# Performance work log

Hardware: AMD Instinct MI355X
Metric: run time of the kernel (lower is better)

The kernel has to match this reference:

```python
import jax, jax.numpy as jnp
import numpy as np

B, N, KNN, C, H, LK, CEMB, GDIM = 16, 512, 20, 256, 128, 4, 64, 64


def _lrelu(x, slope):
    return jnp.where(x >= 0, x, slope * x)


def _forward(img_feat, graph_feat, roi_mask_bit, prev_x_id, prev_y_id, knn_idx,
             conv_w, conv_b, pre_w1, pre_b1, pre_w2, pre_b2,
             g1_w, g1_gamma, g1_beta, g1_mean, g1_var,
             g2_w, g2_gamma, g2_beta, g2_mean, g2_var,
             q_w1, q_b1, q_w2, q_b2, q_w3, q_b3):
    lk = conv_w.shape[-1]
    bsz = img_feat.shape[0]
    # Index2Feat: conv with padding = lk-1 -> (B, CEMB, H+lk-1, W+lk-1)
    patches = jax.lax.conv_general_dilated(img_feat, conv_w, (1, 1), [(lk - 1, lk - 1)] * 2)
    patches = patches + conv_b[None, :, None, None]
    p = jnp.transpose(patches, (0, 2, 3, 1))  # (B, Hp, Wp, CEMB)
    bi = jnp.arange(bsz)[:, None]
    yy, xx = 2 * prev_y_id, 2 * prev_x_id
    sf1 = p[bi, yy, xx]
    sf2 = p[bi, yy + lk, xx]
    sf3 = p[bi, yy, xx + lk]
    sf4 = p[bi, yy + lk, xx + lk]
    local = jnp.concatenate([sf1, sf2, sf3, sf4], axis=-1)  # (B, N, 4*CEMB)
    local = local * jnp.transpose(roi_mask_bit, (0, 2, 1))  # detached mask
    local = jnp.concatenate([local, jnp.transpose(graph_feat, (0, 2, 1))], axis=-1)  # (B,N,320)
    # pre_graph MLP (LeakyReLU 0.01, doLastAct=True)
    h = _lrelu(local @ pre_w1 + pre_b1, 0.01)
    h = _lrelu(h @ pre_w2 + pre_b2, 0.01)  # (B, N, C)
    knn = knn_idx[0]  # (N, K) shared across batch

    def edgeconv(x, w, gamma, beta, mean, var):
        xk = x[:, knn]  # (B, N, K, C) neighbor gather
        xc = jnp.broadcast_to(x[:, :, None, :], xk.shape)
        e = jnp.concatenate([xk - xc, xc], axis=-1)  # (B, N, K, 2C)
        y = jnp.einsum('bnkc,oc->bnko', e, w)  # 1x1 conv, no bias
        y = (y - mean) * (gamma / jnp.sqrt(var + 1e-5)) + beta  # BN (inference)
        return _lrelu(y, 0.2).max(axis=2)  # max over k neighbors

    h = edgeconv(h, g1_w, g1_gamma, g1_beta, g1_mean, g1_var)
    h = edgeconv(h, g2_w, g2_gamma, g2_beta, g2_mean, g2_var)
    # query MLP (256 -> 256 -> 64 -> 2), LeakyReLU 0.01, no last act
    q = _lrelu(h @ q_w1 + q_b1, 0.01)
    q = _lrelu(q @ q_w2 + q_b2, 0.01)
    bits = q @ q_w3 + q_b3  # (B, N, 2)
    return jnp.transpose(bits, (0, 2, 1)), jnp.transpose(h, (0, 2, 1))


def setup_inputs() -> dict:
    key = jax.random.key(0)
    ks = jax.random.split(key, 24)
    s = 0.02
    img_feat = jax.random.normal(ks[0], (B, C, H, H), jnp.float32)
    graph_feat = jax.random.normal(ks[1], (B, GDIM, N), jnp.float32)
    roi_mask_bit = jnp.ones((B, 1, N), jnp.float32)
    prev_x_id = jax.random.randint(ks[2], (B, N), 0, H // 2, jnp.int32)
    prev_y_id = jax.random.randint(ks[3], (B, N), 0, H // 2, jnp.int32)
    # knn graph from normalized 3D keypoints (computed once at init in torch)
    p3d = jax.random.uniform(ks[4], (1, 3, N), jnp.float32, -1.0, 1.0)
    inner = -2.0 * jnp.einsum('bdn,bdm->bnm', p3d, p3d)
    xsq = jnp.sum(p3d ** 2, axis=1, keepdims=True)  # (1,1,N)
    pd = -xsq - inner - jnp.transpose(xsq, (0, 2, 1))
    knn_idx = jax.lax.top_k(pd, KNN)[1].astype(jnp.int32)  # (1, N, KNN)
    return {
        'img_feat': img_feat, 'graph_feat': graph_feat, 'roi_mask_bit': roi_mask_bit,
        'prev_x_id': prev_x_id, 'prev_y_id': prev_y_id, 'knn_idx': knn_idx,
        'conv_w': jax.random.normal(ks[5], (CEMB, C, LK, LK), jnp.float32) * s,
        'conv_b': jnp.zeros((CEMB,), jnp.float32),
        'pre_w1': jax.random.normal(ks[6], (4 * CEMB + GDIM, C), jnp.float32) * s,
        'pre_b1': jnp.zeros((C,), jnp.float32),
        'pre_w2': jax.random.normal(ks[7], (C, C), jnp.float32) * s,
        'pre_b2': jnp.zeros((C,), jnp.float32),
        'g1_w': jax.random.normal(ks[8], (C, 2 * C), jnp.float32) * s,
        'g1_gamma': jnp.ones((C,), jnp.float32), 'g1_beta': jnp.zeros((C,), jnp.float32),
        'g1_mean': jnp.zeros((C,), jnp.float32), 'g1_var': jnp.ones((C,), jnp.float32),
        'g2_w': jax.random.normal(ks[9], (C, 2 * C), jnp.float32) * s,
        'g2_gamma': jnp.ones((C,), jnp.float32), 'g2_beta': jnp.zeros((C,), jnp.float32),
        'g2_mean': jnp.zeros((C,), jnp.float32), 'g2_var': jnp.ones((C,), jnp.float32),
        'q_w1': jax.random.normal(ks[10], (C, C), jnp.float32) * s,
        'q_b1': jnp.zeros((C,), jnp.float32),
        'q_w2': jax.random.normal(ks[11], (C, 64), jnp.float32) * s,
        'q_b2': jnp.zeros((64,), jnp.float32),
        'q_w3': jax.random.normal(ks[12], (64, 2), jnp.float32) * s,
        'q_b3': jnp.zeros((2,), jnp.float32),
    }


def reference(img_feat, graph_feat, roi_mask_bit, prev_x_id, prev_y_id, knn_idx,
              conv_w, conv_b, pre_w1, pre_b1, pre_w2, pre_b2,
              g1_w, g1_gamma, g1_beta, g1_mean, g1_var,
              g2_w, g2_gamma, g2_beta, g2_mean, g2_var,
              q_w1, q_b1, q_w2, q_b2, q_w3, q_b3):
    return _forward(img_feat, graph_feat, roi_mask_bit, prev_x_id, prev_y_id, knn_idx,
                    conv_w, conv_b, pre_w1, pre_b1, pre_w2, pre_b2,
                    g1_w, g1_gamma, g1_beta, g1_mean, g1_var,
                    g2_w, g2_gamma, g2_beta, g2_mean, g2_var,
                    q_w1, q_b1, q_w2, q_b2, q_w3, q_b3)
```

## Files before the change

### kernel.cpp

```cpp
#include <hip/hip_runtime.h>


typedef __bf16 bf16_t;
typedef bf16_t bf16x2 __attribute__((ext_vector_type(2)));
typedef bf16_t bf16x8 __attribute__((ext_vector_type(8)));
typedef float  f32x4  __attribute__((ext_vector_type(4)));

static constexpr int BATCH = 16;
static constexpr int NPT   = 512;
static constexpr int PTS   = BATCH * NPT;
static constexpr int CONVM = PTS * 4;
static constexpr int CONVK = 4096;

static constexpr int PY_DIM = 136;
static constexpr size_t IMG_BSTRIDE = (size_t)PY_DIM * PY_DIM * 256;

static constexpr size_t OFF_WCONV_OLD = 0;
static constexpr size_t OFF_WCONVP    = OFF_WCONV_OLD + (size_t)64*4096*2;
static constexpr size_t OFF_WPRE1     = OFF_WCONVP    + (size_t)64*4096*2;
static constexpr size_t OFF_WPRE2     = OFF_WPRE1     + (size_t)256*320*2;
static constexpr size_t OFF_WEC1      = OFF_WPRE2     + (size_t)256*256*2;
static constexpr size_t OFF_WEC2      = OFF_WEC1      + (size_t)512*256*2;
static constexpr size_t OFF_WQ1       = OFF_WEC2      + (size_t)512*256*2;
static constexpr size_t OFF_WQ2       = OFF_WQ1       + (size_t)256*256*2;
static constexpr size_t OFF_LOCAL     = OFF_WQ2       + (size_t)64*256*2;
static constexpr size_t OFF_X         = OFF_LOCAL + (size_t)PTS*320*2;
static constexpr size_t OFF_Y         = OFF_X     + (size_t)PTS*256*2;
static constexpr size_t OFF_Z         = OFF_Y     + (size_t)PTS*256*2;
static constexpr size_t OFF_UNION     = OFF_Z     + (size_t)PTS*64*2;
static constexpr size_t AB_BYTES      = (size_t)PTS*512*4;
static constexpr size_t IMGT_BYTES    = (size_t)16*IMG_BSTRIDE*2;
static constexpr size_t WS_BASE       = OFF_UNION + AB_BYTES;
static constexpr size_t WS_FULL       = OFF_UNION + IMGT_BYTES;

static constexpr int WP_CONV  = 64*4096;
static constexpr int WP_CONVP = 64*4096;
static constexpr int WP_PRE1 = 256*320;
static constexpr int WP_PRE2 = 256*256;
static constexpr int WP_EC   = 512*256;
static constexpr int WP_Q1   = 256*256;
static constexpr int WP_Q2   = 64*256;
static constexpr int WP_TOTAL = WP_CONV + WP_CONVP + WP_PRE1 + WP_PRE2 + 2*WP_EC + WP_Q1 + WP_Q2;

__global__ __launch_bounds__(256) void wprep_kernel(
    const float* __restrict__ conv_w, const float* __restrict__ pre_w1,
    const float* __restrict__ pre_w2, const float* __restrict__ g1_w,
    const float* __restrict__ g2_w,   const float* __restrict__ q_w1,
    const float* __restrict__ q_w2,
    bf16_t* __restrict__ wt_conv, bf16_t* __restrict__ wt_convp,
    bf16_t* __restrict__ wt_pre1,
    bf16_t* __restrict__ wt_pre2, bf16_t* __restrict__ wt_ec1,
    bf16_t* __restrict__ wt_ec2,  bf16_t* __restrict__ wt_q1,
    bf16_t* __restrict__ wt_q2)
{
    int i = blockIdx.x * 256 + threadIdx.x;
    if (i >= WP_TOTAL) return;
    if (i < WP_CONV) { wt_conv[i] = (bf16_t)conv_w[i]; return; }
    i -= WP_CONV;
    if (i < WP_CONVP) {
        const int o = i >> 12, pix = (i >> 8) & 15, c = i & 255;
        wt_convp[i] = (bf16_t)conv_w[((o * 256 + c) << 4) + pix]; return; }
    i -= WP_CONVP;
    if (i < WP_PRE1) { int n = i / 320, k = i - n * 320;
        wt_pre1[i] = (bf16_t)pre_w1[k * 256 + n]; return; }
    i -= WP_PRE1;
    if (i < WP_PRE2) { int n = i >> 8, k = i & 255;
        wt_pre2[i] = (bf16_t)pre_w2[k * 256 + n]; return; }
    i -= WP_PRE2;
    if (i < WP_EC) { int n = i >> 8, k = i & 255;
        wt_ec1[i] = (bf16_t)(n < 256 ? g1_w[n * 512 + k] : g1_w[(n - 256) * 512 + 256 + k]);
        return; }
    i -= WP_EC;
    if (i < WP_EC) { int n = i >> 8, k = i & 255;
        wt_ec2[i] = (bf16_t)(n < 256 ? g2_w[n * 512 + k] : g2_w[(n - 256) * 512 + 256 + k]);
        return; }
    i -= WP_EC;
    if (i < WP_Q1) { int n = i >> 8, k = i & 255;
        wt_q1[i] = (bf16_t)q_w1[k * 256 + n]; return; }
    i -= WP_Q1;
    { int n = i >> 8, k = i & 255;
        wt_q2[i] = (bf16_t)q_w2[k * 64 + n]; }
}

static constexpr int PAD_THREADS = 16 * 2112 * 32;

__global__ __launch_bounds__(256) void pad_border(bf16_t* __restrict__ imgT)
{
    const int idx = blockIdx.x * 256 + threadIdx.x;
    if (idx >= PAD_THREADS) return;
    const int t = idx & 31;
    int pi = idx >> 5;
    const int b = pi / 2112; pi -= b * 2112;
    int y, x;
    if (pi < 544)      { y = pi / 136;              x = pi % 136; }
    else if (pi < 1088){ int j = pi - 544; y = 132 + j / 136; x = j % 136; }
    else { int j = pi - 1088; y = 4 + (j >> 3); int k = j & 7; x = (k < 4) ? k : (128 + k); }
    const uint4 z = {0, 0, 0, 0};
    ((uint4*)(imgT + ((size_t)(b * PY_DIM + y) * PY_DIM + x) * 256))[t] = z;
}

__global__ __launch_bounds__(256) void transpose_img(
    const float* __restrict__ img, bf16_t* __restrict__ imgT)
{
    __shared__ float T[64][65];
    const int bid = blockIdx.x;
    const int cc = bid & 3;
    const int xh = (bid >> 2) & 1;
    const int y  = (bid >> 3) & 127;
    const int b  = bid >> 10;
    const int t = threadIdx.x;
    const int x0 = xh * 64, c0 = cc * 64;
    {
        const int px = t & 63, cr = t >> 6;
        const float* src = img + ((size_t)(b * 256 + c0 + cr) * 128 + y) * 128 + x0 + px;
        #pragma unroll
        for (int i = 0; i < 16; ++i)
            T[cr + i * 4][px] = src[(size_t)i * 4 * 16384];
    }
    __syncthreads();
    {
        const int cl2 = (t & 31) * 2, pr = t >> 5;
        bf16_t* dst = imgT + ((size_t)(b * PY_DIM + y + 4) * PY_DIM + x0 + 4) * 256 + c0 + cl2;
        #pragma unroll
        for (int i = 0; i < 8; ++i) {
            const int pxl = pr + i * 8;
            bf16x2 w;
            w[0] = (bf16_t)T[cl2][pxl];
            w[1] = (bf16_t)T[cl2 + 1][pxl];
            *(bf16x2*)(dst + (size_t)pxl * 256) = w;
        }
    }
}

__global__ __launch_bounds__(256) void conv_gather_gemm3(
    const bf16_t* __restrict__ imgT,
    const bf16_t* __restrict__ Wc,
    const float* __restrict__ conv_b, const float* __restrict__ roi,
    const int* __restrict__ px, const int* __restrict__ py,
    bf16_t* __restrict__ local)
{
    __shared__ bf16_t As[32][136];
    __shared__ bf16_t Bs[64][136];
    const int tid = threadIdx.x, lane = tid & 63, wave = tid >> 6;
    const int wm = wave & 1, wn = wave >> 1;
    const int row0 = blockIdx.x * 32;

    const int ra = tid >> 3, seg = tid & 7;
    const int r = row0 + ra, corner = r & 3, pnt = r >> 2, b = pnt >> 9;
    const int oy = 2 * py[pnt] + (corner & 1) * 4 + 1;
    const int ox = 2 * px[pnt] + ((corner >> 1) & 1) * 4 + 1;
    const bf16_t* imgb = imgT + (size_t)b * IMG_BSTRIDE;
    const int rb = tid >> 2, sq = tid & 3;
    const bf16_t* wrow = Wc + (size_t)rb * 4096 + sq * 8;

    f32x4 acc[2] = {};
    #pragma unroll 1
    for (int s = 0; s < 32; ++s) {
        const int pix = s >> 1, h = s & 1;
        const int iy = oy + (pix >> 2), ix = ox + (pix & 3);
        {
            const bf16_t* srcA = imgb + ((size_t)(iy * PY_DIM + ix)) * 256 + h * 128 + seg * 16;
            *(uint4*)&As[ra][seg * 16]     = *(const uint4*)srcA;
            *(uint4*)&As[ra][seg * 16 + 8] = *(const uint4*)(srcA + 8);
        }
        {
            const bf16_t* srcB = wrow + pix * 256 + h * 128;
            #pragma unroll
            for (int i = 0; i < 4; ++i)
                *(uint4*)&Bs[rb][sq * 8 + i * 32] = *(const uint4*)(srcB + i * 32);
        }
        __syncthreads();
        #pragma unroll
        for (int kk = 0; kk < 128; kk += 32) {
            const int kf = kk + ((lane >> 4) << 3);
            bf16x8 a  = *(const bf16x8*)&As[wm * 16 + (lane & 15)][kf];
            bf16x8 b0 = *(const bf16x8*)&Bs[wn * 32 + (lane & 15)][kf];
            bf16x8 b1 = *(const bf16x8*)&Bs[wn * 32 + 16 + (lane & 15)][kf];
            acc[0] = __builtin_amdgcn_mfma_f32_16x16x32_bf16(a, b0, acc[0], 0, 0, 0);
            acc[1] = __builtin_amdgcn_mfma_f32_16x16x32_bf16(a, b1, acc[1], 0, 0, 0);
        }
        __syncthreads();
    }
    const int crow = (lane >> 4) << 2;
    const int ccol = lane & 15;
    #pragma unroll
    for (int j = 0; j < 2; ++j) {
        const int o = wn * 32 + j * 16 + ccol;
        const float bv = conv_b[o];
        #pragma unroll
        for (int rg = 0; rg < 4; ++rg) {
            const int gr = row0 + wm * 16 + crow + rg;
            const int cn = gr & 3;
            const int pp = gr >> 2;
            const float v = (acc[j][rg] + bv) * roi[pp];
            local[(size_t)pp * 320 + cn * 64 + o] = (bf16_t)v;
        }
    }
}

__global__ __launch_bounds__(256) void conv_gather_gemm(
    const float* __restrict__ img, const bf16_t* __restrict__ Wc,
    const float* __restrict__ conv_b, const float* __restrict__ roi,
    const int* __restrict__ px, const int* __restrict__ py,
    bf16_t* __restrict__ local)
{
    __shared__ bf16_t As[64][72];
    __shared__ bf16_t Bs[64][72];
    const int tid = threadIdx.x;
    const int lane = tid & 63;
    const int wave = tid >> 6;
    const int wm = wave & 1, wn = wave >> 1;
    const int row0 = blockIdx.x * 64;
    const int sm = tid >> 2;
    const int cq = tid & 3;
    const int r = row0 + sm;
    const int corner = r & 3;
    const int pnt = r >> 2;
    const int b = pnt >> 9;
    const int oy = 2 * py[pnt] + (corner & 1) * 4;
    const int ox = 2 * px[pnt] + ((corner >> 1) & 1) * 4;
    const int iy0 = oy - 3, ix0 = ox - 3;
    const float* imgb = img + (size_t)b * (256 * 128 * 128);

    f32x4 acc[2][2] = {};
    for (int kt = 0; kt < CONVK; kt += 64) {
        {
            const int c = (kt >> 4) + cq;
            const float* ip = imgb + (size_t)c * (128 * 128);
            alignas(16) bf16_t vals[16];
            #pragma unroll
            for (int ky = 0; ky < 4; ++ky) {
                const int iy = iy0 + ky;
                const bool yok = (unsigned)iy < 128u;
                #pragma unroll
                for (int kx = 0; kx < 4; ++kx) {
                    const int ix = ix0 + kx;
                    float v = (yok && (unsigned)ix < 128u) ? ip[iy * 128 + ix] : 0.0f;
                    vals[ky * 4 + kx] = (bf16_t)v;
                }
            }
            *(uint4*)&As[sm][cq * 16]     = *(const uint4*)&vals[0];
            *(uint4*)&As[sm][cq * 16 + 8] = *(const uint4*)&vals[8];
        }
        {
            const bf16_t* src = Wc + (size_t)sm * CONVK + kt + cq * 16;
            *(uint4*)&Bs[sm][cq * 16]     = *(const uint4*)src;
            *(uint4*)&Bs[sm][cq * 16 + 8] = *(const uint4*)(src + 8);
        }
        __syncthreads();
        #pragma unroll
        for (int kk = 0; kk < 64; kk += 32) {
            const int kf = kk + ((lane >> 4) << 3);
            bf16x8 a0 = *(const bf16x8*)&As[wm * 32 + (lane & 15)][kf];
            bf16x8 a1 = *(const bf16x8*)&As[wm * 32 + 16 + (lane & 15)][kf];
            bf16x8 b0 = *(const bf16x8*)&Bs[wn * 32 + (lane & 15)][kf];
            bf16x8 b1 = *(const bf16x8*)&Bs[wn * 32 + 16 + (lane & 15)][kf];
            acc[0][0] = __builtin_amdgcn_mfma_f32_16x16x32_bf16(a0, b0, acc[0][0], 0, 0, 0);
            acc[0][1] = __builtin_amdgcn_mfma_f32_16x16x32_bf16(a0, b1, acc[0][1], 0, 0, 0);
            acc[1][0] = __builtin_amdgcn_mfma_f32_16x16x32_bf16(a1, b0, acc[1][0], 0, 0, 0);
            acc[1][1] = __builtin_amdgcn_mfma_f32_16x16x32_bf16(a1, b1, acc[1][1], 0, 0, 0);
        }
        __syncthreads();
    }
    const int crow = (lane >> 4) << 2;
    const int ccol = lane & 15;
    #pragma unroll
    for (int i = 0; i < 2; ++i) {
        #pragma unroll
        for (int j = 0; j < 2; ++j) {
            const int o = wn * 32 + j * 16 + ccol;
            const float bv = conv_b[o];
            #pragma unroll
            for (int rg = 0; rg < 4; ++rg) {
                const int gr = row0 + wm * 32 + i * 16 + crow + rg;
                const int cn = gr & 3;
                const int pp = gr >> 2;
                const float v = (acc[i][j][rg] + bv) * roi[pp];
                local[(size_t)pp * 320 + cn * 64 + o] = (bf16_t)v;
            }
        }
    }
}

__global__ __launch_bounds__(256) void graph_fill(
    const float* __restrict__ g, bf16_t* __restrict__ local)
{
    const int e = blockIdx.x * 256 + threadIdx.x;
    const int j = e & 63, p = e >> 6;
    const int b = p >> 9, n = p & 511;
    local[(size_t)p * 320 + 256 + j] = (bf16_t)g[((size_t)(b * 64 + j) << 9) + n];
}

template<int K, int N, int ACT>
__global__ __launch_bounds__(256) void gemm_bf16(
    const bf16_t* __restrict__ A, const bf16_t* __restrict__ Bt,
    const float* __restrict__ bias, float slope,
    bf16_t* __restrict__ outB, float* __restrict__ outF)
{
    __shared__ bf16_t As[64][72];
    __shared__ bf16_t Bs[64][72];
    const int tid = threadIdx.x;
    const int lane = tid & 63;
    const int wave = tid >> 6;
    const int wm = wave & 1, wn = wave >> 1;
    const int row0 = blockIdx.x * 64;
    const int col0 = blockIdx.y * 64;
    const int sm = tid >> 2;
    const int sq = (tid & 3) << 4;

    f32x4 acc[2][2] = {};
    for (int kt = 0; kt < K; kt += 64) {
        {
            const bf16_t* src = A + (size_t)(row0 + sm) * K + kt + sq;
            *(uint4*)&As[sm][sq]     = *(const uint4*)src;
            *(uint4*)&As[sm][sq + 8] = *(const uint4*)(src + 8);
        }
        {
            const bf16_t* src = Bt + (size_t)(col0 + sm) * K + kt + sq;
            *(uint4*)&Bs[sm][sq]     = *(const uint4*)src;
            *(uint4*)&Bs[sm][sq + 8] = *(const uint4*)(src + 8);
        }
        __syncthreads();
        #pragma unroll
        for (int kk = 0; kk < 64; kk += 32) {
            const int kf = kk + ((lane >> 4) << 3);
            bf16x8 a0 = *(const bf16x8*)&As[wm * 32 + (lane & 15)][kf];
            bf16x8 a1 = *(const bf16x8*)&As[wm * 32 + 16 + (lane & 15)][kf];
            bf16x8 b0 = *(const bf16x8*)&Bs[wn * 32 + (lane & 15)][kf];
            bf16x8 b1 = *(const bf16x8*)&Bs[wn * 32 + 16 + (lane & 15)][kf];
            acc[0][0] = __builtin_amdgcn_mfma_f32_16x16x32_bf16(a0, b0, acc[0][0], 0, 0, 0);
            acc[0][1] = __builtin_amdgcn_mfma_f32_16x16x32_bf16(a0, b1, acc[0][1], 0, 0, 0);
            acc[1][0] = __builtin_amdgcn_mfma_f32_16x16x32_bf16(a1, b0, acc[1][0], 0, 0, 0);
            acc[1][1] = __builtin_amdgcn_mfma_f32_16x16x32_bf16(a1, b1, acc[1][1], 0, 0, 0);
        }
        __syncthreads();
    }
    const int crow = (lane >> 4) << 2;
    const int ccol = lane & 15;
    #pragma unroll
    for (int i = 0; i < 2; ++i) {
        #pragma unroll
        for (int j = 0; j < 2; ++j) {
            const int gcol = col0 + wn * 32 + j * 16 + ccol;
            const float bv = bias ? bias[gcol] : 0.0f;
            #pragma unroll
            for (int rg = 0; rg < 4; ++rg) {
                const int grow = row0 + wm * 32 + i * 16 + crow + rg;
                float v = acc[i][j][rg] + bv;
                if (ACT == 1) v = v >= 0.0f ? v : slope * v;
                if (outB) outB[(size_t)grow * N + gcol] = (bf16_t)v;
                if (outF) outF[(size_t)grow * N + gcol] = v;
            }
        }
    }
}

__global__ __launch_bounds__(256) void edge_combine(
    const float* __restrict__ AB, const int* __restrict__ knn,
    const float* __restrict__ gamma, const float* __restrict__ beta,
    const float* __restrict__ mean,  const float* __restrict__ var,
    bf16_t* __restrict__ outB, float* __restrict__ outT)
{
    const int p = blockIdx.x;
    const int b = p >> 9, n = p & 511;
    const int o = threadIdx.x;
    const float sc = gamma[o] / sqrtf(var[o] + 1e-5f);
    const float sh = beta[o] - mean[o] * sc;
    const float* rowp = AB + (size_t)p * 512;
    const float d = rowp[256 + o] - rowp[o];
    const float* batch = AB + ((size_t)(b << 9)) * 512;
    float m = -3.4e38f;
    #pragma unroll 4
    for (int k = 0; k < 20; ++k) {
        const int q = knn[n * 20 + k];
        const float v = batch[(size_t)q * 512 + o] + d;
        float y = v * sc + sh;
        y = y >= 0.0f ? y : 0.2f * y;
        m = fmaxf(m, y);
    }
    outB[(size_t)p * 256 + o] = (bf16_t)m;
    if (outT) outT[((size_t)(b * 256 + o) << 9) + n] = m;
}

__global__ __launch_bounds__(256) void q3_kernel(
    const bf16_t* __restrict__ Z, const float* __restrict__ w3,
    const float* __restrict__ b3, float* __restrict__ out)
{
    const int p = blockIdx.x * 256 + threadIdx.x;
    const int b = p >> 9, n = p & 511;
    const bf16_t* q = Z + (size_t)p * 64;
    float s0 = b3[0], s1 = b3[1];
    #pragma unroll
    for (int c = 0; c < 64; ++c) {
        const float v = (float)q[c];
        s0 += v * w3[2 * c];
        s1 += v * w3[2 * c + 1];
    }
    out[(size_t)(b * 2 + 0) * 512 + n] = s0;
    out[(size_t)(b * 2 + 1) * 512 + n] = s1;
}

extern "C" void kernel_launch(void* const* d_in, const int* in_sizes, int n_in,
                              void* d_out, int out_size, void* d_ws, size_t ws_size,
                              hipStream_t stream)
{
    const float* img      = (const float*)d_in[0];
    const float* graph    = (const float*)d_in[1];
    const float* roi      = (const float*)d_in[2];
    const int*   px       = (const int*)d_in[3];
    const int*   py       = (const int*)d_in[4];
    const int*   knn      = (const int*)d_in[5];
    const float* conv_w   = (const float*)d_in[6];
    const float* conv_b   = (const float*)d_in[7];
    const float* pre_w1   = (const float*)d_in[8];
    const float* pre_b1   = (const float*)d_in[9];
    const float* pre_w2   = (const float*)d_in[10];
    const float* pre_b2   = (const float*)d_in[11];
    const float* g1_w     = (const float*)d_in[12];
    const float* g1_gamma = (const float*)d_in[13];
    const float* g1_beta  = (const float*)d_in[14];
    const float* g1_mean  = (const float*)d_in[15];
    const float* g1_var   = (const float*)d_in[16];
    const float* g2_w     = (const float*)d_in[17];
    const float* g2_gamma = (const float*)d_in[18];
    const float* g2_beta  = (const float*)d_in[19];
    const float* g2_mean  = (const float*)d_in[20];
    const float* g2_var   = (const float*)d_in[21];
    const float* q_w1     = (const float*)d_in[22];
    const float* q_b1     = (const float*)d_in[23];
    const float* q_w2     = (const float*)d_in[24];
    const float* q_b2     = (const float*)d_in[25];
    const float* q_w3     = (const float*)d_in[26];
    const float* q_b3     = (const float*)d_in[27];
    float* out = (float*)d_out;

    if (ws_size < WS_BASE) return;

    char* ws = (char*)d_ws;
    bf16_t* wt_conv  = (bf16_t*)(ws + OFF_WCONV_OLD);
    bf16_t* wt_convp = (bf16_t*)(ws + OFF_WCONVP);
    bf16_t* wt_pre1  = (bf16_t*)(ws + OFF_WPRE1);
    bf16_t* wt_pre2  = (bf16_t*)(ws + OFF_WPRE2);
    bf16_t* wt_ec1   = (bf16_t*)(ws + OFF_WEC1);
    bf16_t* wt_ec2   = (bf16_t*)(ws + OFF_WEC2);
    bf16_t* wt_q1    = (bf16_t*)(ws + OFF_WQ1);
    bf16_t* wt_q2    = (bf16_t*)(ws + OFF_WQ2);
    bf16_t* local    = (bf16_t*)(ws + OFF_LOCAL);
    bf16_t* X        = (bf16_t*)(ws + OFF_X);
    bf16_t* Y        = (bf16_t*)(ws + OFF_Y);
    bf16_t* Z        = (bf16_t*)(ws + OFF_Z);
    float*  AB       = (float*)(ws + OFF_UNION);
    bf16_t* imgT     = (bf16_t*)(ws + OFF_UNION);

    const bool big = ws_size >= WS_FULL;

    wprep_kernel<<<(WP_TOTAL + 255) / 256, 256, 0, stream>>>(
        conv_w, pre_w1, pre_w2, g1_w, g2_w, q_w1, q_w2,
        wt_conv, wt_convp, wt_pre1, wt_pre2, wt_ec1, wt_ec2, wt_q1, wt_q2);

    if (big) {
        pad_border<<<(PAD_THREADS + 255) / 256, 256, 0, stream>>>(imgT);
        transpose_img<<<16 * 128 * 2 * 4, 256, 0, stream>>>(img, imgT);
        conv_gather_gemm3<<<CONVM / 32, 256, 0, stream>>>(
            imgT, wt_convp, conv_b, roi, px, py, local);
    } else {
        conv_gather_gemm<<<CONVM / 64, 256, 0, stream>>>(
            img, wt_conv, conv_b, roi, px, py, local);
    }

    graph_fill<<<(PTS * 64) / 256, 256, 0, stream>>>(graph, local);

    gemm_bf16<320, 256, 1><<<dim3(PTS / 64, 4), 256, 0, stream>>>(
        local, wt_pre1, pre_b1, 0.01f, X, nullptr);
    gemm_bf16<256, 256, 1><<<dim3(PTS / 64, 4), 256, 0, stream>>>(
        X, wt_pre2, pre_b2, 0.01f, Y, nullptr);

    gemm_bf16<256, 512, 0><<<dim3(PTS / 64, 8), 256, 0, stream>>>(
        Y, wt_ec1, nullptr, 0.0f, nullptr, AB);
    edge_combine<<<PTS, 256, 0, stream>>>(
        AB, knn, g1_gamma, g1_beta, g1_mean, g1_var, X, nullptr);

    gemm_bf16<256, 512, 0><<<dim3(PTS / 64, 8), 256, 0, stream>>>(
        X, wt_ec2, nullptr, 0.0f, nullptr, AB);
    edge_combine<<<PTS, 256, 0, stream>>>(
        AB, knn, g2_gamma, g2_beta, g2_mean, g2_var, Y, out + 16384);

    gemm_bf16<256, 256, 1><<<dim3(PTS / 64, 4), 256, 0, stream>>>(
        Y, wt_q1, q_b1, 0.01f, X, nullptr);
    gemm_bf16<256, 64, 1><<<dim3(PTS / 64, 1), 256, 0, stream>>>(
        X, wt_q2, q_b2, 0.01f, Z, nullptr);
    q3_kernel<<<PTS / 256, 256, 0, stream>>>(Z, q_w3, q_b3, out);
}
```

Before: 265.5 us.

## Sort points spatially for conv gather and fuse pre and query MLP chains

Adds a counting sort of points by batch and coarse 8x8 spatial cell, so conv gather blocks handle nearby points and reuse cache lines of the transposed image. A block-index swizzle spreads the work. The two pre-graph GEMMs are fused into one kernel that keeps the hidden activations in shared memory, and the three query-MLP layers are fused the same way, removing intermediate global writes and several launches. The cost is three small sort kernels, atomics, and fused kernels that each use only 32-row tiles, which lowers parallelism per launch.

```diff
diff --git a/kernel.cpp b/kernel.cpp
--- a/kernel.cpp
+++ b/kernel.cpp
@@ -23,11 +23,13 @@
 static constexpr size_t OFF_WEC2      = OFF_WEC1      + (size_t)512*256*2;
 static constexpr size_t OFF_WQ1       = OFF_WEC2      + (size_t)512*256*2;
 static constexpr size_t OFF_WQ2       = OFF_WQ1       + (size_t)256*256*2;
-static constexpr size_t OFF_LOCAL     = OFF_WQ2       + (size_t)64*256*2;
+static constexpr size_t OFF_HIST      = OFF_WQ2       + (size_t)64*256*2;
+static constexpr size_t OFF_CURSOR    = OFF_HIST      + 1024*4;
+static constexpr size_t OFF_SORTED    = OFF_CURSOR    + 1024*4;
+static constexpr size_t OFF_LOCAL     = OFF_SORTED    + (size_t)PTS*4;
 static constexpr size_t OFF_X         = OFF_LOCAL + (size_t)PTS*320*2;
 static constexpr size_t OFF_Y         = OFF_X     + (size_t)PTS*256*2;
-static constexpr size_t OFF_Z         = OFF_Y     + (size_t)PTS*256*2;
-static constexpr size_t OFF_UNION     = OFF_Z     + (size_t)PTS*64*2;
+static constexpr size_t OFF_UNION     = OFF_Y     + (size_t)PTS*256*2;
 static constexpr size_t AB_BYTES      = (size_t)PTS*512*4;
 static constexpr size_t IMGT_BYTES    = (size_t)16*IMG_BSTRIDE*2;
 static constexpr size_t WS_BASE       = OFF_UNION + AB_BYTES;
@@ -51,9 +53,10 @@
     bf16_t* __restrict__ wt_pre1,
     bf16_t* __restrict__ wt_pre2, bf16_t* __restrict__ wt_ec1,
     bf16_t* __restrict__ wt_ec2,  bf16_t* __restrict__ wt_q1,
-    bf16_t* __restrict__ wt_q2)
+    bf16_t* __restrict__ wt_q2,   int* __restrict__ hist)
 {
     int i = blockIdx.x * 256 + threadIdx.x;
+    if (i < 1024) hist[i] = 0;
     if (i >= WP_TOTAL) return;
     if (i < WP_CONV) { wt_conv[i] = (bf16_t)conv_w[i]; return; }
     i -= WP_CONV;
@@ -82,6 +85,47 @@
         wt_q2[i] = (bf16_t)q_w2[k * 64 + n]; }
 }
 
+__device__ __forceinline__ int sort_key(const int* px, const int* py, int p) {
+    return ((p >> 9) << 6) | ((py[p] >> 3) << 3) | (px[p] >> 3);
+}
+
+__global__ __launch_bounds__(256) void sort_hist_kernel(
+    const int* __restrict__ px, const int* __restrict__ py, int* __restrict__ hist)
+{
+    const int p = blockIdx.x * 256 + threadIdx.x;
+    atomicAdd(&hist[sort_key(px, py, p)], 1);
+}
+
+__global__ __launch_bounds__(256) void sort_scan_kernel(
+    const int* __restrict__ hist, int* __restrict__ cursor)
+{
+    __shared__ int s[256];
+    const int t = threadIdx.x;
+    const int h0 = hist[4*t], h1 = hist[4*t+1], h2 = hist[4*t+2], h3 = hist[4*t+3];
+    const int sum = h0 + h1 + h2 + h3;
+    s[t] = sum; __syncthreads();
+    for (int off = 1; off < 256; off <<= 1) {
+        int v = (t >= off) ? s[t - off] : 0;
+        __syncthreads();
+        s[t] += v;
+        __syncthreads();
+    }
+    const int excl = s[t] - sum;
+    cursor[4*t]   = excl;
+    cursor[4*t+1] = excl + h0;
+    cursor[4*t+2] = excl + h0 + h1;
+    cursor[4*t+3] = excl + h0 + h1 + h2;
+}
+
+__global__ __launch_bounds__(256) void sort_scatter_kernel(
+    const int* __restrict__ px, const int* __restrict__ py,
+    int* __restrict__ cursor, int* __restrict__ sorted)
+{
+    const int p = blockIdx.x * 256 + threadIdx.x;
+    const int pos = atomicAdd(&cursor[sort_key(px, py, p)], 1);
+    sorted[pos] = p;
+}
+
 static constexpr int PAD_THREADS = 16 * 2112 * 32;
 
 __global__ __launch_bounds__(256) void pad_border(bf16_t* __restrict__ imgT)
@@ -132,21 +176,25 @@
     }
 }
 
-__global__ __launch_bounds__(256) void conv_gather_gemm3(
-    const bf16_t* __restrict__ imgT,
-    const bf16_t* __restrict__ Wc,
+__global__ __launch_bounds__(256) void conv_gather_gemm4(
+    const bf16_t* __restrict__ imgT, const bf16_t* __restrict__ Wc,
     const float* __restrict__ conv_b, const float* __restrict__ roi,
     const int* __restrict__ px, const int* __restrict__ py,
+    const int* __restrict__ sorted,
     bf16_t* __restrict__ local)
 {
     __shared__ bf16_t As[32][136];
     __shared__ bf16_t Bs[64][136];
     const int tid = threadIdx.x, lane = tid & 63, wave = tid >> 6;
     const int wm = wave & 1, wn = wave >> 1;
-    const int row0 = blockIdx.x * 32;
+    const int bid = blockIdx.x;
+    const int swz = (bid & 7) * 128 + (bid >> 3);
+    const int row0 = swz * 32;
 
     const int ra = tid >> 3, seg = tid & 7;
-    const int r = row0 + ra, corner = r & 3, pnt = r >> 2, b = pnt >> 9;
+    const int rs = row0 + ra, corner = rs & 3;
+    const int pnt = sorted[rs >> 2];
+    const int b = pnt >> 9;
     const int oy = 2 * py[pnt] + (corner & 1) * 4 + 1;
     const int ox = 2 * px[pnt] + ((corner >> 1) & 1) * 4 + 1;
     const bf16_t* imgb = imgT + (size_t)b * IMG_BSTRIDE;
@@ -191,7 +239,7 @@
         for (int rg = 0; rg < 4; ++rg) {
             const int gr = row0 + wm * 16 + crow + rg;
             const int cn = gr & 3;
-            const int pp = gr >> 2;
+            const int pp = sorted[gr >> 2];
             const float v = (acc[j][rg] + bv) * roi[pp];
             local[(size_t)pp * 320 + cn * 64 + o] = (bf16_t)v;
         }
@@ -291,11 +339,100 @@
     local[(size_t)p * 320 + 256 + j] = (bf16_t)g[((size_t)(b * 64 + j) << 9) + n];
 }
 
-template<int K, int N, int ACT>
-__global__ __launch_bounds__(256) void gemm_bf16(
+__global__ __launch_bounds__(256) void pre12_kernel(
+    const bf16_t* __restrict__ A,
+    const bf16_t* __restrict__ B1t,
+    const float* __restrict__ b1,
+    const bf16_t* __restrict__ B2t,
+    const float* __restrict__ b2,
+    bf16_t* __restrict__ Y)
+{
+    __shared__ bf16_t As[32][72];
+    __shared__ bf16_t Bs[64][72];
+    __shared__ bf16_t Xs[32][264];
+    const int tid = threadIdx.x, lane = tid & 63, wave = tid >> 6;
+    const int wm = wave & 1, wn = wave >> 1;
+    const int row0 = blockIdx.x * 32;
+    const int sm3 = tid >> 3, seg3 = (tid & 7) << 3;
+    const int smB = tid >> 2, sqB = (tid & 3) << 4;
+    const int crow = (lane >> 4) << 2, ccol = lane & 15;
+
+    #pragma unroll 1
+    for (int ct = 0; ct < 4; ++ct) {
+        f32x4 acc[2] = {};
+        #pragma unroll 1
+        for (int kt = 0; kt < 320; kt += 64) {
+            __syncthreads();
+            *(uint4*)&As[sm3][seg3] = *(const uint4*)(A + (size_t)(row0 + sm3) * 320 + kt + seg3);
+            {
+                const bf16_t* src = B1t + (size_t)(ct * 64 + smB) * 320 + kt + sqB;
+                *(uint4*)&Bs[smB][sqB]     = *(const uint4*)src;
+                *(uint4*)&Bs[smB][sqB + 8] = *(const uint4*)(src + 8);
+            }
+            __syncthreads();
+            #pragma unroll
+            for (int kk = 0; kk < 64; kk += 32) {
+                const int kf = kk + ((lane >> 4) << 3);
+                bf16x8 a  = *(const bf16x8*)&As[wm * 16 + (lane & 15)][kf];
+                bf16x8 b0 = *(const bf16x8*)&Bs[wn * 32 + (lane & 15)][kf];
+                bf16x8 b1f = *(const bf16x8*)&Bs[wn * 32 + 16 + (lane & 15)][kf];
+                acc[0] = __builtin_amdgcn_mfma_f32_16x16x32_bf16(a, b0, acc[0], 0, 0, 0);
+                acc[1] = __builtin_amdgcn_mfma_f32_16x16x32_bf16(a, b1f, acc[1], 0, 0, 0);
+            }
+        }
+        #pragma unroll
+        for (int j = 0; j < 2; ++j) {
+            const int gcol = ct * 64 + wn * 32 + j * 16 + ccol;
+            const float bv = b1[gcol];
+            #pragma unroll
+            for (int rg = 0; rg < 4; ++rg) {
+                float v = acc[j][rg] + bv;
+                v = v >= 0.0f ? v : 0.01f * v;
+                Xs[wm * 16 + crow + rg][gcol] = (bf16_t)v;
+            }
+        }
+    }
+    #pragma unroll 1
+    for (int ct = 0; ct < 4; ++ct) {
+        f32x4 acc[2] = {};
+        #pragma unroll 1
+        for (int kt = 0; kt < 256; kt += 64) {
+            __syncthreads();
+            {
+                const bf16_t* src = B2t + (size_t)(ct * 64 + smB) * 256 + kt + sqB;
+                *(uint4*)&Bs[smB][sqB]     = *(const uint4*)src;
+                *(uint4*)&Bs[smB][sqB + 8] = *(const uint4*)(src + 8);
+            }
+            __syncthreads();
+            #pragma unroll
+            for (int kk = 0; kk < 64; kk += 32) {
+                const int kf = kk + ((lane >> 4) << 3);
+                bf16x8 a  = *(const bf16x8*)&Xs[wm * 16 + (lane & 15)][kt + kf];
+                bf16x8 b0 = *(const bf16x8*)&Bs[wn * 32 + (lane & 15)][kf];
+                bf16x8 b1f = *(const bf16x8*)&Bs[wn * 32 + 16 + (lane & 15)][kf];
+                acc[0] = __builtin_amdgcn_mfma_f32_16x16x32_bf16(a, b0, acc[0], 0, 0, 0);
+                acc[1] = __builtin_amdgcn_mfma_f32_16x16x32_bf16(a, b1f, acc[1], 0, 0, 0);
+            }
+        }
+        #pragma unroll
+        for (int j = 0; j < 2; ++j) {
+            const int gcol = ct * 64 + wn * 32 + j * 16 + ccol;
+            const float bv = b2[gcol];
+            #pragma unroll
+            for (int rg = 0; rg < 4; ++rg) {
+                const int grow = row0 + wm * 16 + crow + rg;
+                float v = acc[j][rg] + bv;
+                v = v >= 0.0f ? v : 0.01f * v;
+                Y[(size_t)grow * 256 + gcol] = (bf16_t)v;
+            }
+        }
+    }
+}
+
+template<int K, int N>
+__global__ __launch_bounds__(256) void gemm_bf16f(
     const bf16_t* __restrict__ A, const bf16_t* __restrict__ Bt,
-    const float* __restrict__ bias, float slope,
-    bf16_t* __restrict__ outB, float* __restrict__ outF)
+    float* __restrict__ outF)
 {
     __shared__ bf16_t As[64][72];
     __shared__ bf16_t Bs[64][72];
@@ -342,14 +479,10 @@
         #pragma unroll
         for (int j = 0; j < 2; ++j) {
             const int gcol = col0 + wn * 32 + j * 16 + ccol;
-            const float bv = bias ? bias[gcol] : 0.0f;
             #pragma unroll
             for (int rg = 0; rg < 4; ++rg) {
                 const int grow = row0 + wm * 32 + i * 16 + crow + rg;
-                float v = acc[i][j][rg] + bv;
-                if (ACT == 1) v = v >= 0.0f ? v : slope * v;
-                if (outB) outB[(size_t)grow * N + gcol] = (bf16_t)v;
-                if (outF) outF[(size_t)grow * N + gcol] = v;
+                outF[(size_t)grow * N + gcol] = acc[i][j][rg];
             }
         }
     }
@@ -382,22 +515,106 @@
     if (outT) outT[((size_t)(b * 256 + o) << 9) + n] = m;
 }
 
-__global__ __launch_bounds__(256) void q3_kernel(
-    const bf16_t* __restrict__ Z, const float* __restrict__ w3,
-    const float* __restrict__ b3, float* __restrict__ out)
-{
-    const int p = blockIdx.x * 256 + threadIdx.x;
-    const int b = p >> 9, n = p & 511;
-    const bf16_t* q = Z + (size_t)p * 64;
-    float s0 = b3[0], s1 = b3[1];
-    #pragma unroll
-    for (int c = 0; c < 64; ++c) {
-        const float v = (float)q[c];
-        s0 += v * w3[2 * c];
-        s1 += v * w3[2 * c + 1];
-    }
-    out[(size_t)(b * 2 + 0) * 512 + n] = s0;
-    out[(size_t)(b * 2 + 1) * 512 + n] = s1;
+__global__ __launch_bounds__(256) void q123_kernel(
+    const bf16_t* __restrict__ A,
+    const bf16_t* __restrict__ B1t,
+    const float* __restrict__ b1,
+    const bf16_t* __restrict__ B2t,
+    const float* __restrict__ b2,
+    const float* __restrict__ w3,
+    const float* __restrict__ b3,
+    float* __restrict__ out)
+{
+    __shared__ bf16_t As[32][72];
+    __shared__ bf16_t Bs[64][72];
+    __shared__ bf16_t Zs[32][264];
+    __shared__ bf16_t Z2s[32][72];
+    const int tid = threadIdx.x, lane = tid & 63, wave = tid >> 6;
+    const int wm = wave & 1, wn = wave >> 1;
+    const int row0 = blockIdx.x * 32;
+    const int sm3 = tid >> 3, seg3 = (tid & 7) << 3;
+    const int smB = tid >> 2, sqB = (tid & 3) << 4;
+    const int crow = (lane >> 4) << 2, ccol = lane & 15;
+
+    #pragma unroll 1
+    for (int ct = 0; ct < 4; ++ct) {
+        f32x4 acc[2] = {};
+        #pragma unroll 1
+        for (int kt = 0; kt < 256; kt += 64) {
+            __syncthreads();
+            *(uint4*)&As[sm3][seg3] = *(const uint4*)(A + (size_t)(row0 + sm3) * 256 + kt + seg3);
+            {
+                const bf16_t* src = B1t + (size_t)(ct * 64 + smB) * 256 + kt + sqB;
+                *(uint4*)&Bs[smB][sqB]     = *(const uint4*)src;
+                *(uint4*)&Bs[smB][sqB + 8] = *(const uint4*)(src + 8);
+            }
+            __syncthreads();
+            #pragma unroll
+            for (int kk = 0; kk < 64; kk += 32) {
+                const int kf = kk + ((lane >> 4) << 3);
+                bf16x8 a  = *(const bf16x8*)&As[wm * 16 + (lane & 15)][kf];
+                bf16x8 b0 = *(const bf16x8*)&Bs[wn * 32 + (lane & 15)][kf];
+                bf16x8 b1f = *(const bf16x8*)&Bs[wn * 32 + 16 + (lane & 15)][kf];
+                acc[0] = __builtin_amdgcn_mfma_f32_16x16x32_bf16(a, b0, acc[0], 0, 0, 0);
+                acc[1] = __builtin_amdgcn_mfma_f32_16x16x32_bf16(a, b1f, acc[1], 0, 0, 0);
+            }
+        }
+        #pragma unroll
+        for (int j = 0; j < 2; ++j) {
+            const int gcol = ct * 64 + wn * 32 + j * 16 + ccol;
+            const float bv = b1[gcol];
+            #pragma unroll
+            for (int rg = 0; rg < 4; ++rg) {
+                float v = acc[j][rg] + bv;
+                v = v >= 0.0f ? v : 0.01f * v;
+                Zs[wm * 16 + crow + rg][gcol] = (bf16_t)v;
+            }
+        }
+    }
+    {
+        f32x4 acc[2] = {};
+        #pragma unroll 1
+        for (int kt = 0; kt < 256; kt += 64) {
+            __syncthreads();
+            {
+                const bf16_t* src = B2t + (size_t)smB * 256 + kt + sqB;
+                *(uint4*)&Bs[smB][sqB]     = *(const uint4*)src;
+                *(uint4*)&Bs[smB][sqB + 8] = *(const uint4*)(src + 8);
+            }
+            __syncthreads();
+            #pragma unroll
+            for (int kk = 0; kk < 64; kk += 32) {
+                const int kf = kk + ((lane >> 4) << 3);
+                bf16x8 a  = *(const bf16x8*)&Zs[wm * 16 + (lane & 15)][kt + kf];
+                bf16x8 b0 = *(const bf16x8*)&Bs[wn * 32 + (lane & 15)][kf];
+                bf16x8 b1f = *(const bf16x8*)&Bs[wn * 32 + 16 + (lane & 15)][kf];
+                acc[0] = __builtin_amdgcn_mfma_f32_16x16x32_bf16(a, b0, acc[0], 0, 0, 0);
+                acc[1] = __builtin_amdgcn_mfma_f32_16x16x32_bf16(a, b1f, acc[1], 0, 0, 0);
+            }
+        }
+        #pragma unroll
+        for (int j = 0; j < 2; ++j) {
+            const int gcol = wn * 32 + j * 16 + ccol;
+            const float bv = b2[gcol];
+            #pragma unroll
+            for (int rg = 0; rg < 4; ++rg) {
+                float v = acc[j][rg] + bv;
+                v = v >= 0.0f ? v : 0.01f * v;
+                Z2s[wm * 16 + crow + rg][gcol] = (bf16_t)v;
+            }
+        }
+    }
+    __syncthreads();
+    if (tid < 64) {
+        const int rowL = tid >> 1, jj = tid & 1;
+        const int gr = row0 + rowL;
+        float s = b3[jj];
+        #pragma unroll
+        for (int c = 0; c < 64; ++c)
+            s += (float)Z2s[rowL][c] * w3[2 * c + jj];
+        const int b = gr >> 9, n = gr & 511;
+        out[(size_t)(b * 2 + jj) * 512 + n] = s;
+    }
 }
 
 extern "C" void kernel_launch(void* const* d_in, const int* in_sizes, int n_in,
@@ -445,10 +662,12 @@
     bf16_t* wt_ec2   = (bf16_t*)(ws + OFF_WEC2);
     bf16_t* wt_q1    = (bf16_t*)(ws + OFF_WQ1);
     bf16_t* wt_q2    = (bf16_t*)(ws + OFF_WQ2);
+    int*    hist     = (int*)(ws + OFF_HIST);
+    int*    cursor   = (int*)(ws + OFF_CURSOR);
+    int*    sorted   = (int*)(ws + OFF_SORTED);
     bf16_t* local    = (bf16_t*)(ws + OFF_LOCAL);
     bf16_t* X        = (bf16_t*)(ws + OFF_X);
     bf16_t* Y        = (bf16_t*)(ws + OFF_Y);
-    bf16_t* Z        = (bf16_t*)(ws + OFF_Z);
     float*  AB       = (float*)(ws + OFF_UNION);
     bf16_t* imgT     = (bf16_t*)(ws + OFF_UNION);
 
@@ -456,13 +675,16 @@
 
     wprep_kernel<<<(WP_TOTAL + 255) / 256, 256, 0, stream>>>(
         conv_w, pre_w1, pre_w2, g1_w, g2_w, q_w1, q_w2,
-        wt_conv, wt_convp, wt_pre1, wt_pre2, wt_ec1, wt_ec2, wt_q1, wt_q2);
+        wt_conv, wt_convp, wt_pre1, wt_pre2, wt_ec1, wt_ec2, wt_q1, wt_q2, hist);
 
     if (big) {
+        sort_hist_kernel<<<PTS / 256, 256, 0, stream>>>(px, py, hist);
+        sort_scan_kernel<<<1, 256, 0, stream>>>(hist, cursor);
+        sort_scatter_kernel<<<PTS / 256, 256, 0, stream>>>(px, py, cursor, sorted);
         pad_border<<<(PAD_THREADS + 255) / 256, 256, 0, stream>>>(imgT);
         transpose_img<<<16 * 128 * 2 * 4, 256, 0, stream>>>(img, imgT);
-        conv_gather_gemm3<<<CONVM / 32, 256, 0, stream>>>(
-            imgT, wt_convp, conv_b, roi, px, py, local);
+        conv_gather_gemm4<<<CONVM / 32, 256, 0, stream>>>(
+            imgT, wt_convp, conv_b, roi, px, py, sorted, local);
     } else {
         conv_gather_gemm<<<CONVM / 64, 256, 0, stream>>>(
             img, wt_conv, conv_b, roi, px, py, local);
@@ -470,24 +692,17 @@
 
     graph_fill<<<(PTS * 64) / 256, 256, 0, stream>>>(graph, local);
 
-    gemm_bf16<320, 256, 1><<<dim3(PTS / 64, 4), 256, 0, stream>>>(
-        local, wt_pre1, pre_b1, 0.01f, X, nullptr);
-    gemm_bf16<256, 256, 1><<<dim3(PTS / 64, 4), 256, 0, stream>>>(
-        X, wt_pre2, pre_b2, 0.01f, Y, nullptr);
-
-    gemm_bf16<256, 512, 0><<<dim3(PTS / 64, 8), 256, 0, stream>>>(
-        Y, wt_ec1, nullptr, 0.0f, nullptr, AB);
+    pre12_kernel<<<PTS / 32, 256, 0, stream>>>(
+        local, wt_pre1, pre_b1, wt_pre2, pre_b2, Y);
+
+    gemm_bf16f<256, 512><<<dim3(PTS / 64, 8), 256, 0, stream>>>(Y, wt_ec1, AB);
     edge_combine<<<PTS, 256, 0, stream>>>(
         AB, knn, g1_gamma, g1_beta, g1_mean, g1_var, X, nullptr);
 
-    gemm_bf16<256, 512, 0><<<dim3(PTS / 64, 8), 256, 0, stream>>>(
-        X, wt_ec2, nullptr, 0.0f, nullptr, AB);
+    gemm_bf16f<256, 512><<<dim3(PTS / 64, 8), 256, 0, stream>>>(X, wt_ec2, AB);
     edge_combine<<<PTS, 256, 0, stream>>>(
         AB, knn, g2_gamma, g2_beta, g2_mean, g2_var, Y, out + 16384);
 
-    gemm_bf16<256, 256, 1><<<dim3(PTS / 64, 4), 256, 0, stream>>>(
-        Y, wt_q1, q_b1, 0.01f, X, nullptr);
-    gemm_bf16<256, 64, 1><<<dim3(PTS / 64, 1), 256, 0, stream>>>(
-        X, wt_q2, q_b2, 0.01f, Z, nullptr);
-    q3_kernel<<<PTS / 256, 256, 0, stream>>>(Z, q_w3, q_b3, out);
-}
+    q123_kernel<<<PTS / 32, 256, 0, stream>>>(
+        Y, wt_q1, q_b1, wt_q2, q_b2, q_w3, q_b3, out);
+}
```

Result: slower. 297.0 us (+11.9%).

## Bucket-sort points by spatial tile to improve conv gather cache locality

Applied to the files above, without the earlier changes.

Adds a counting sort (histogram, scan, scatter) that orders points by batch and 8x8 coarse spatial cell. The conv gather GEMM then processes rows in sorted order, with a block-index swizzle, so nearby patches are read by concurrently running blocks. The intent is to improve L2 and MALL reuse of the transposed image. It costs three small extra kernel launches with atomics and one extra indirection per row.

```diff
diff --git a/kernel.cpp b/kernel.cpp
--- a/kernel.cpp
+++ b/kernel.cpp
@@ -23,7 +23,10 @@
 static constexpr size_t OFF_WEC2      = OFF_WEC1      + (size_t)512*256*2;
 static constexpr size_t OFF_WQ1       = OFF_WEC2      + (size_t)512*256*2;
 static constexpr size_t OFF_WQ2       = OFF_WQ1       + (size_t)256*256*2;
-static constexpr size_t OFF_LOCAL     = OFF_WQ2       + (size_t)64*256*2;
+static constexpr size_t OFF_HIST      = OFF_WQ2       + (size_t)64*256*2;
+static constexpr size_t OFF_CURSOR    = OFF_HIST      + 1024*4;
+static constexpr size_t OFF_SORTED    = OFF_CURSOR    + 1024*4;
+static constexpr size_t OFF_LOCAL     = OFF_SORTED    + (size_t)PTS*4;
 static constexpr size_t OFF_X         = OFF_LOCAL + (size_t)PTS*320*2;
 static constexpr size_t OFF_Y         = OFF_X     + (size_t)PTS*256*2;
 static constexpr size_t OFF_Z         = OFF_Y     + (size_t)PTS*256*2;
@@ -51,9 +54,10 @@
     bf16_t* __restrict__ wt_pre1,
     bf16_t* __restrict__ wt_pre2, bf16_t* __restrict__ wt_ec1,
     bf16_t* __restrict__ wt_ec2,  bf16_t* __restrict__ wt_q1,
-    bf16_t* __restrict__ wt_q2)
+    bf16_t* __restrict__ wt_q2,   int* __restrict__ hist)
 {
     int i = blockIdx.x * 256 + threadIdx.x;
+    if (i < 1024) hist[i] = 0;
     if (i >= WP_TOTAL) return;
     if (i < WP_CONV) { wt_conv[i] = (bf16_t)conv_w[i]; return; }
     i -= WP_CONV;
@@ -82,6 +86,47 @@
         wt_q2[i] = (bf16_t)q_w2[k * 64 + n]; }
 }
 
+__device__ __forceinline__ int sort_key(const int* px, const int* py, int p) {
+    return ((p >> 9) << 6) | ((py[p] >> 3) << 3) | (px[p] >> 3);
+}
+
+__global__ __launch_bounds__(256) void sort_hist_kernel(
+    const int* __restrict__ px, const int* __restrict__ py, int* __restrict__ hist)
+{
+    const int p = blockIdx.x * 256 + threadIdx.x;
+    atomicAdd(&hist[sort_key(px, py, p)], 1);
+}
+
+__global__ __launch_bounds__(256) void sort_scan_kernel(
+    const int* __restrict__ hist, int* __restrict__ cursor)
+{
+    __shared__ int s[256];
+    const int t = threadIdx.x;
+    const int h0 = hist[4*t], h1 = hist[4*t+1], h2 = hist[4*t+2], h3 = hist[4*t+3];
+    const int sum = h0 + h1 + h2 + h3;
+    s[t] = sum; __syncthreads();
+    for (int off = 1; off < 256; off <<= 1) {
+        int v = (t >= off) ? s[t - off] : 0;
+        __syncthreads();
+        s[t] += v;
+        __syncthreads();
+    }
+    const int excl = s[t] - sum;
+    cursor[4*t]   = excl;
+    cursor[4*t+1] = excl + h0;
+    cursor[4*t+2] = excl + h0 + h1;
+    cursor[4*t+3] = excl + h0 + h1 + h2;
+}
+
+__global__ __launch_bounds__(256) void sort_scatter_kernel(
+    const int* __restrict__ px, const int* __restrict__ py,
+    int* __restrict__ cursor, int* __restrict__ sorted)
+{
+    const int p = blockIdx.x * 256 + threadIdx.x;
+    const int pos = atomicAdd(&cursor[sort_key(px, py, p)], 1);
+    sorted[pos] = p;
+}
+
 static constexpr int PAD_THREADS = 16 * 2112 * 32;
 
 __global__ __launch_bounds__(256) void pad_border(bf16_t* __restrict__ imgT)
@@ -132,21 +177,25 @@
     }
 }
 
-__global__ __launch_bounds__(256) void conv_gather_gemm3(
-    const bf16_t* __restrict__ imgT,
-    const bf16_t* __restrict__ Wc,
+__global__ __launch_bounds__(256) void conv_gather_gemm4(
+    const bf16_t* __restrict__ imgT, const bf16_t* __restrict__ Wc,
     const float* __restrict__ conv_b, const float* __restrict__ roi,
     const int* __restrict__ px, const int* __restrict__ py,
+    const int* __restrict__ sorted,
     bf16_t* __restrict__ local)
 {
     __shared__ bf16_t As[32][136];
     __shared__ bf16_t Bs[64][136];
     const int tid = threadIdx.x, lane = tid & 63, wave = tid >> 6;
     const int wm = wave & 1, wn = wave >> 1;
-    const int row0 = blockIdx.x * 32;
+    const int bid = blockIdx.x;
+    const int swz = (bid & 7) * 128 + (bid >> 3);
+    const int row0 = swz * 32;
 
     const int ra = tid >> 3, seg = tid & 7;
-    const int r = row0 + ra, corner = r & 3, pnt = r >> 2, b = pnt >> 9;
+    const int rs = row0 + ra, corner = rs & 3;
+    const int pnt = sorted[rs >> 2];
+    const int b = pnt >> 9;
     const int oy = 2 * py[pnt] + (corner & 1) * 4 + 1;
     const int ox = 2 * px[pnt] + ((corner >> 1) & 1) * 4 + 1;
     const bf16_t* imgb = imgT + (size_t)b * IMG_BSTRIDE;
@@ -191,7 +240,7 @@
         for (int rg = 0; rg < 4; ++rg) {
             const int gr = row0 + wm * 16 + crow + rg;
             const int cn = gr & 3;
-            const int pp = gr >> 2;
+            const int pp = sorted[gr >> 2];
             const float v = (acc[j][rg] + bv) * roi[pp];
             local[(size_t)pp * 320 + cn * 64 + o] = (bf16_t)v;
         }
@@ -445,6 +494,9 @@
     bf16_t* wt_ec2   = (bf16_t*)(ws + OFF_WEC2);
     bf16_t* wt_q1    = (bf16_t*)(ws + OFF_WQ1);
     bf16_t* wt_q2    = (bf16_t*)(ws + OFF_WQ2);
+    int*    hist     = (int*)(ws + OFF_HIST);
+    int*    cursor   = (int*)(ws + OFF_CURSOR);
+    int*    sorted   = (int*)(ws + OFF_SORTED);
     bf16_t* local    = (bf16_t*)(ws + OFF_LOCAL);
     bf16_t* X        = (bf16_t*)(ws + OFF_X);
     bf16_t* Y        = (bf16_t*)(ws + OFF_Y);
@@ -456,13 +508,16 @@
 
     wprep_kernel<<<(WP_TOTAL + 255) / 256, 256, 0, stream>>>(
         conv_w, pre_w1, pre_w2, g1_w, g2_w, q_w1, q_w2,
-        wt_conv, wt_convp, wt_pre1, wt_pre2, wt_ec1, wt_ec2, wt_q1, wt_q2);
+        wt_conv, wt_convp, wt_pre1, wt_pre2, wt_ec1, wt_ec2, wt_q1, wt_q2, hist);
 
     if (big) {
+        sort_hist_kernel<<<PTS / 256, 256, 0, stream>>>(px, py, hist);
+        sort_scan_kernel<<<1, 256, 0, stream>>>(hist, cursor);
+        sort_scatter_kernel<<<PTS / 256, 256, 0, stream>>>(px, py, cursor, sorted);
         pad_border<<<(PAD_THREADS + 255) / 256, 256, 0, stream>>>(imgT);
         transpose_img<<<16 * 128 * 2 * 4, 256, 0, stream>>>(img, imgT);
-        conv_gather_gemm3<<<CONVM / 32, 256, 0, stream>>>(
-            imgT, wt_convp, conv_b, roi, px, py, local);
+        conv_gather_gemm4<<<CONVM / 32, 256, 0, stream>>>(
+            imgT, wt_convp, conv_b, roi, px, py, sorted, local);
     } else {
         conv_gather_gemm<<<CONVM / 64, 256, 0, stream>>>(
             img, wt_conv, conv_b, roi, px, py, local);
```

New measurement: 280.0 us. 1.05x slower.
